# Kernel optimization log

Measured on AMD Instinct MI355X. Metric: run time of the kernel, lower is better.

The kernel has to match this reference:

```python
import jax, jax.numpy as jnp
import numpy as np

N, C, K, M = 100000, 128, 27, 4  # voxels, channels, 3^3 kernel offsets, branches
EPS = 1e-5


def setup_inputs() -> dict:
    key = jax.random.key(0)
    ks = jax.random.split(key, 4)
    x = jax.random.normal(ks[0], (N, C), jnp.float32)
    # neighbor index per voxel per kernel offset (Minkowski kernel map)
    nbr_idx = jax.random.randint(ks[1], (N, K), 0, N, dtype=jnp.int32)
    W1 = jax.random.normal(ks[2], (M, C, C), jnp.float32) * (1.0 / np.sqrt(C))
    g1 = jnp.ones((M, C), jnp.float32)
    b1 = jnp.zeros((M, C), jnp.float32)
    wk = jax.random.normal(ks[3], (M, K, C), jnp.float32) * (1.0 / np.sqrt(K))
    g_out = jnp.ones((C,), jnp.float32)
    b_out = jnp.zeros((C,), jnp.float32)
    return {"x": x, "nbr_idx": nbr_idx, "W1": W1, "g1": g1, "b1": b1,
            "wk": wk, "g_out": g_out, "b_out": b_out}


def _bn(h, g, b):
    # training-mode batch norm over the voxel axis
    mu = h.mean(0)
    var = h.var(0)
    return (h - mu) * jax.lax.rsqrt(var + EPS) * g + b


def reference(x, nbr_idx, W1, g1, b1, wk, g_out, b_out):
    out = jnp.zeros_like(x)
    for m in range(M):  # fixed small branch count
        # Conv1x1 (pointwise) + BN + ReLU
        h = jax.nn.relu(_bn(x @ W1[m], g1[m], b1[m]))  # [N, C]
        # channelwise 3^3 sparse conv: gather neighbor, per-channel scale, accumulate
        acc = jnp.zeros_like(h)
        for k in range(K):  # fixed 27 kernel offsets; avoids [N,K,C] materialization
            acc = acc + h[nbr_idx[:, k]] * wk[m, k]
        out = out + acc  # stack(-1).sum(-1) over branches
    out = jax.nn.relu(_bn(out, g_out, b_out))  # out_bn_relu
    out = out + x  # residual (inplanes == planes)
    return jax.nn.relu(out)  # final nonlinearity ('ReLU')
```

## Files before the change

### kernel.cpp

```cpp
#include <hip/hip_runtime.h>

#define KK 27
#define EPSV 1e-5f

typedef __attribute__((ext_vector_type(8))) short bf16x8;
typedef __attribute__((ext_vector_type(4))) float f32x4;
typedef __attribute__((ext_vector_type(4))) unsigned int u32x4;

static __device__ __forceinline__ unsigned short f2bf(float f) {
    unsigned u = __float_as_uint(f);
    u = u + 0x7fffu + ((u >> 16) & 1u);
    return (unsigned short)(u >> 16);
}
static __device__ __forceinline__ float bflo(unsigned u) { return __uint_as_float(u << 16); }
static __device__ __forceinline__ float bfhi(unsigned u) { return __uint_as_float(u & 0xffff0000u); }

__global__ void k0_wt(const float* __restrict__ W1, unsigned short* __restrict__ WT) {
    int m = blockIdx.x >> 7, n = blockIdx.x & 127, k = threadIdx.x;
    WT[((m * 128 + n) * 128) + k] = f2bf(W1[(m * 128 + k) * 128 + n]);
}

__launch_bounds__(256)
__global__ void kA_gemm(const float* __restrict__ x, const unsigned short* __restrict__ WT,
                        unsigned short* __restrict__ Yall, float* __restrict__ ysum,
                        float* __restrict__ ysq, int N, int m0, int m1, int ystride) {
    __shared__ unsigned short As[64 * 136];
    __shared__ unsigned short Bs[128 * 136];
    const int t = threadIdx.x;
    const int i0 = blockIdx.x * 64;

#pragma unroll
    for (int it = 0; it < 8; ++it) {
        int flat = it * 256 + t;
        int r = flat >> 5, c4 = (flat & 31) * 4;
        float4 v = make_float4(0.f, 0.f, 0.f, 0.f);
        if (i0 + r < N) v = *(const float4*)(x + (size_t)(i0 + r) * 128 + c4);
        ushort4 bb;
        bb.x = f2bf(v.x); bb.y = f2bf(v.y); bb.z = f2bf(v.z); bb.w = f2bf(v.w);
        *(ushort4*)(As + r * 136 + c4) = bb;
    }

    const int w = t >> 6, lane = t & 63;
    const int wr = w >> 1, wc = w & 1;
    const int r16 = lane & 15, q = lane >> 4;

    for (int m = m0; m < m1; ++m) {
        __syncthreads();
        const uint4* Wp = (const uint4*)(WT + (size_t)m * 128 * 128);
#pragma unroll
        for (int it = 0; it < 8; ++it) {
            int flat = it * 256 + t;
            int n = flat >> 4, kc = flat & 15;
            uint4 v = Wp[n * 16 + kc];
            *(uint4*)(Bs + n * 136 + kc * 8) = v;
        }
        __syncthreads();

        f32x4 acc[2][4];
#pragma unroll
        for (int a = 0; a < 2; ++a)
#pragma unroll
            for (int b = 0; b < 4; ++b) { acc[a][b][0] = 0.f; acc[a][b][1] = 0.f; acc[a][b][2] = 0.f; acc[a][b][3] = 0.f; }

#pragma unroll
        for (int ks = 0; ks < 4; ++ks) {
            int ko = ks * 32 + q * 8;
            bf16x8 af[2], bfr[4];
#pragma unroll
            for (int ri = 0; ri < 2; ++ri)
                af[ri] = *(const bf16x8*)(As + (wr * 32 + ri * 16 + r16) * 136 + ko);
#pragma unroll
            for (int ci = 0; ci < 4; ++ci)
                bfr[ci] = *(const bf16x8*)(Bs + (wc * 64 + ci * 16 + r16) * 136 + ko);
#pragma unroll
            for (int ri = 0; ri < 2; ++ri)
#pragma unroll
                for (int ci = 0; ci < 4; ++ci)
                    acc[ri][ci] = __builtin_amdgcn_mfma_f32_16x16x32_bf16(af[ri], bfr[ci], acc[ri][ci], 0, 0, 0);
        }

#pragma unroll
        for (int ci = 0; ci < 4; ++ci) {
            float s = 0.f, s2 = 0.f;
#pragma unroll
            for (int ri = 0; ri < 2; ++ri) {
#pragma unroll
                for (int r = 0; r < 4; ++r) {
                    int row = i0 + wr * 32 + ri * 16 + q * 4 + r;
                    float vv = acc[ri][ci][r];
                    if (row < N) { s += vv; s2 += vv * vv; }
                }
            }
            s  += __shfl_xor(s, 16);  s  += __shfl_xor(s, 32);
            s2 += __shfl_xor(s2, 16); s2 += __shfl_xor(s2, 32);
            if (lane < 16) {
                int col = wc * 64 + ci * 16 + r16;
                atomicAdd(ysum + m * 128 + col, s);
                atomicAdd(ysq  + m * 128 + col, s2);
            }
        }

        __syncthreads();
        unsigned short* Ys = Bs;
#pragma unroll
        for (int ci = 0; ci < 4; ++ci) {
            int col = wc * 64 + ci * 16 + r16;
#pragma unroll
            for (int ri = 0; ri < 2; ++ri) {
#pragma unroll
                for (int r = 0; r < 4; ++r) {
                    int rl = wr * 32 + ri * 16 + q * 4 + r;
                    Ys[rl * 136 + col] = f2bf(acc[ri][ci][r]);
                }
            }
        }
        __syncthreads();
        const int cb = (m - m0) * 128;
#pragma unroll
        for (int it = 0; it < 4; ++it) {
            int chunk = it * 256 + t;
            int row = chunk >> 4, c8 = (chunk & 15) * 8;
            if (i0 + row < N) {
                u32x4 v = *(const u32x4*)(Ys + row * 136 + c8);
                __builtin_nontemporal_store(v, (u32x4*)(Yall + (size_t)(i0 + row) * ystride + cb + c8));
            }
        }
    }
}

__global__ void k2_coef(const float* __restrict__ ysum, const float* __restrict__ ysq,
                        const float* __restrict__ g1, const float* __restrict__ b1,
                        float* __restrict__ a1, float* __restrict__ c1, int N, int m0) {
    int c = threadIdx.x & 127;
    int m = m0 + (threadIdx.x >> 7);
    float mean = ysum[m * 128 + c] / (float)N;
    float var  = ysq[m * 128 + c] / (float)N - mean * mean;
    float a = g1[m * 128 + c] * rsqrtf(var + EPSV);
    a1[m * 128 + c] = a;
    c1[m * 128 + c] = b1[m * 128 + c] - mean * a;
}

__launch_bounds__(256)
__global__ void k4_all(const unsigned short* __restrict__ Yall, const int* __restrict__ nbr,
                       const float* __restrict__ wkg, const float* __restrict__ a1,
                       const float* __restrict__ c1, float* __restrict__ P,
                       float* __restrict__ osum, float* __restrict__ osq, int N) {
    __shared__ unsigned short wkL[4 * KK * 136];
    __shared__ float ssum[128], ssq[128];
    const int t = threadIdx.x;
    for (int idx = t; idx < 4 * KK * 128; idx += 256) {
        int c = idx & 127, km = idx >> 7;
        wkL[km * 136 + c] = f2bf(wkg[idx]);
    }
    if (t < 128) { ssum[t] = 0.f; ssq[t] = 0.f; }

    const int lane = t & 63;
    const int m = lane >> 4, c16 = lane & 15;

    float Ar[8], Cr[8];
    {
        const float4 A0 = *(const float4*)(a1 + m * 128 + c16 * 8);
        const float4 A1 = *(const float4*)(a1 + m * 128 + c16 * 8 + 4);
        const float4 C0 = *(const float4*)(c1 + m * 128 + c16 * 8);
        const float4 C1 = *(const float4*)(c1 + m * 128 + c16 * 8 + 4);
        Ar[0]=A0.x; Ar[1]=A0.y; Ar[2]=A0.z; Ar[3]=A0.w;
        Ar[4]=A1.x; Ar[5]=A1.y; Ar[6]=A1.z; Ar[7]=A1.w;
        Cr[0]=C0.x; Cr[1]=C0.y; Cr[2]=C0.z; Cr[3]=C0.w;
        Cr[4]=C1.x; Cr[5]=C1.y; Cr[6]=C1.z; Cr[7]=C1.w;
    }
    __syncthreads();

    float os[8], oq[8];
#pragma unroll
    for (int e = 0; e < 8; ++e) { os[e] = 0.f; oq[e] = 0.f; }

    const int wid = blockIdx.x * 4 + (t >> 6);
    const int nw  = gridDim.x * 4;
    for (int vox = wid; vox < N; vox += nw) {
        const int sv = __builtin_amdgcn_readfirstlane(vox);
        const int* np = nbr + (size_t)sv * KK;
        float acc[8];
#pragma unroll
        for (int e = 0; e < 8; ++e) acc[e] = 0.f;

#pragma unroll 3
        for (int k = 0; k < KK; ++k) {
            const int j = np[k];
            const uint4 hv = *(const uint4*)(Yall + ((size_t)j << 9) + lane * 8);
            const uint4 wv = *(const uint4*)(wkL + (m * KK + k) * 136 + c16 * 8);
            float h0 = fmaxf(0.f, bflo(hv.x) * Ar[0] + Cr[0]);
            float h1 = fmaxf(0.f, bfhi(hv.x) * Ar[1] + Cr[1]);
            float h2 = fmaxf(0.f, bflo(hv.y) * Ar[2] + Cr[2]);
            float h3 = fmaxf(0.f, bfhi(hv.y) * Ar[3] + Cr[3]);
            float h4 = fmaxf(0.f, bflo(hv.z) * Ar[4] + Cr[4]);
            float h5 = fmaxf(0.f, bfhi(hv.z) * Ar[5] + Cr[5]);
            float h6 = fmaxf(0.f, bflo(hv.w) * Ar[6] + Cr[6]);
            float h7 = fmaxf(0.f, bfhi(hv.w) * Ar[7] + Cr[7]);
            acc[0] += h0 * bflo(wv.x); acc[1] += h1 * bfhi(wv.x);
            acc[2] += h2 * bflo(wv.y); acc[3] += h3 * bfhi(wv.y);
            acc[4] += h4 * bflo(wv.z); acc[5] += h5 * bfhi(wv.z);
            acc[6] += h6 * bflo(wv.w); acc[7] += h7 * bfhi(wv.w);
        }

#pragma unroll
        for (int e = 0; e < 8; ++e) {
            acc[e] += __shfl_xor(acc[e], 16);
            acc[e] += __shfl_xor(acc[e], 32);
        }

        if (lane < 16) {
            f32x4 v0 = {acc[0], acc[1], acc[2], acc[3]};
            f32x4 v1 = {acc[4], acc[5], acc[6], acc[7]};
            float* p = P + (size_t)vox * 128 + c16 * 8;
            __builtin_nontemporal_store(v0, (f32x4*)p);
            __builtin_nontemporal_store(v1, (f32x4*)(p + 4));
#pragma unroll
            for (int e = 0; e < 8; ++e) { os[e] += acc[e]; oq[e] += acc[e] * acc[e]; }
        }
    }

    if (lane < 16) {
#pragma unroll
        for (int e = 0; e < 8; ++e) {
            atomicAdd(ssum + c16 * 8 + e, os[e]);
            atomicAdd(ssq  + c16 * 8 + e, oq[e]);
        }
    }
    __syncthreads();
    if (t < 128) {
        atomicAdd(osum + t, ssum[t]);
        atomicAdd(osq  + t, ssq[t]);
    }
}

template <int MODE>
__launch_bounds__(256)
__global__ void k4_gather(const unsigned short* __restrict__ Ym, int ystride,
                          const int* __restrict__ nbr,
                          const float* __restrict__ wkm, const float* __restrict__ a1m,
                          const float* __restrict__ c1m, float* __restrict__ P,
                          float* __restrict__ osum, float* __restrict__ osq, int N) {
    __shared__ float wkL[KK * 132];
    __shared__ float ssum[128], ssq[128];
    const int t = threadIdx.x;
    for (int idx = t; idx < KK * 128; idx += 256) {
        int k = idx >> 7, c = idx & 127;
        wkL[k * 132 + c] = wkm[k * 128 + c];
    }
    if (MODE == 2) { if (t < 128) { ssum[t] = 0.f; ssq[t] = 0.f; } }

    const int w = t >> 6, lane = t & 63;
    const int q = lane >> 4, c16 = lane & 15;
    const int slot = w * 4 + q;
    const int vox = blockIdx.x * 16 + slot;
    const bool alive = vox < N;

    float aR[8], cR[8];
    {
        const float4 A0 = *(const float4*)(a1m + c16 * 8);
        const float4 A1 = *(const float4*)(a1m + c16 * 8 + 4);
        const float4 C0 = *(const float4*)(c1m + c16 * 8);
        const float4 C1 = *(const float4*)(c1m + c16 * 8 + 4);
        aR[0]=A0.x; aR[1]=A0.y; aR[2]=A0.z; aR[3]=A0.w;
        aR[4]=A1.x; aR[5]=A1.y; aR[6]=A1.z; aR[7]=A1.w;
        cR[0]=C0.x; cR[1]=C0.y; cR[2]=C0.z; cR[3]=C0.w;
        cR[4]=C1.x; cR[5]=C1.y; cR[6]=C1.z; cR[7]=C1.w;
    }
    __syncthreads();

    const long long base = alive ? (long long)vox * KK : 0;
    float acc[8];
#pragma unroll
    for (int e = 0; e < 8; ++e) acc[e] = 0.f;

#pragma unroll 3
    for (int k = 0; k < KK; ++k) {
        int j = nbr[base + k];
        const uint4 hv = *(const uint4*)(Ym + (size_t)j * ystride + c16 * 8);
        const float4 wa = *(const float4*)(wkL + k * 132 + c16 * 8);
        const float4 wb = *(const float4*)(wkL + k * 132 + c16 * 8 + 4);
        float h0 = fmaxf(0.f, bflo(hv.x) * aR[0] + cR[0]);
        float h1 = fmaxf(0.f, bfhi(hv.x) * aR[1] + cR[1]);
        float h2 = fmaxf(0.f, bflo(hv.y) * aR[2] + cR[2]);
        float h3 = fmaxf(0.f, bfhi(hv.y) * aR[3] + cR[3]);
        float h4 = fmaxf(0.f, bflo(hv.z) * aR[4] + cR[4]);
        float h5 = fmaxf(0.f, bfhi(hv.z) * aR[5] + cR[5]);
        float h6 = fmaxf(0.f, bflo(hv.w) * aR[6] + cR[6]);
        float h7 = fmaxf(0.f, bfhi(hv.w) * aR[7] + cR[7]);
        acc[0] += h0 * wa.x; acc[1] += h1 * wa.y;
        acc[2] += h2 * wa.z; acc[3] += h3 * wa.w;
        acc[4] += h4 * wb.x; acc[5] += h5 * wb.y;
        acc[6] += h6 * wb.z; acc[7] += h7 * wb.w;
    }

    float os[8], oq[8];
    if (alive) {
        float* p = P + (size_t)vox * 128 + c16 * 8;
        if (MODE == 0) {
            float4 v0 = {acc[0], acc[1], acc[2], acc[3]};
            float4 v1 = {acc[4], acc[5], acc[6], acc[7]};
            *(float4*)p = v0;
            *(float4*)(p + 4) = v1;
        } else {
            float4 o0 = *(const float4*)p, o1 = *(const float4*)(p + 4);
            o0.x += acc[0]; o0.y += acc[1]; o0.z += acc[2]; o0.w += acc[3];
            o1.x += acc[4]; o1.y += acc[5]; o1.z += acc[6]; o1.w += acc[7];
            *(float4*)p = o0;
            *(float4*)(p + 4) = o1;
            if (MODE == 2) {
                os[0] = o0.x; oq[0] = o0.x * o0.x;
                os[1] = o0.y; oq[1] = o0.y * o0.y;
                os[2] = o0.z; oq[2] = o0.z * o0.z;
                os[3] = o0.w; oq[3] = o0.w * o0.w;
                os[4] = o1.x; oq[4] = o1.x * o1.x;
                os[5] = o1.y; oq[5] = o1.y * o1.y;
                os[6] = o1.z; oq[6] = o1.z * o1.z;
                os[7] = o1.w; oq[7] = o1.w * o1.w;
            }
        }
    }
    if (MODE == 2) {
        if (!alive) {
#pragma unroll
            for (int e = 0; e < 8; ++e) { os[e] = 0.f; oq[e] = 0.f; }
        }
#pragma unroll
        for (int e = 0; e < 8; ++e) {
            os[e] += __shfl_xor(os[e], 16); os[e] += __shfl_xor(os[e], 32);
            oq[e] += __shfl_xor(oq[e], 16); oq[e] += __shfl_xor(oq[e], 32);
        }
        if (lane < 16) {
#pragma unroll
            for (int e = 0; e < 8; ++e) {
                atomicAdd(ssum + c16 * 8 + e, os[e]);
                atomicAdd(ssq  + c16 * 8 + e, oq[e]);
            }
        }
        __syncthreads();
        if (t < 128) {
            atomicAdd(osum + t, ssum[t]);
            atomicAdd(osq  + t, ssq[t]);
        }
    }
}

__global__ void k5_coef(const float* __restrict__ osum, const float* __restrict__ osq,
                        const float* __restrict__ g, const float* __restrict__ b,
                        float* __restrict__ ao, float* __restrict__ co, int N) {
    int c = threadIdx.x;
    float mean = osum[c] / (float)N;
    float var  = osq[c] / (float)N - mean * mean;
    float a = g[c] * rsqrtf(var + EPSV);
    ao[c] = a;
    co[c] = b[c] - mean * a;
}

__launch_bounds__(256)
__global__ void k6_final(float* __restrict__ P, const float* __restrict__ x,
                         const float* __restrict__ ao, const float* __restrict__ co, int N) {
    long long t4 = ((long long)blockIdx.x * 256 + threadIdx.x) * 4;
    if (t4 >= (long long)N * 128) return;
    int c4 = (int)(t4 & 127);
    float4 p  = *(const float4*)(P + t4);
    float4 xv = *(const float4*)(x + t4);
    float4 a  = *(const float4*)(ao + c4);
    float4 c  = *(const float4*)(co + c4);
    float4 o;
    o.x = fmaxf(0.f, fmaxf(0.f, p.x * a.x + c.x) + xv.x);
    o.y = fmaxf(0.f, fmaxf(0.f, p.y * a.y + c.y) + xv.y);
    o.z = fmaxf(0.f, fmaxf(0.f, p.z * a.z + c.z) + xv.z);
    o.w = fmaxf(0.f, fmaxf(0.f, p.w * a.w + c.w) + xv.w);
    *(float4*)(P + t4) = o;
}

extern "C" void kernel_launch(void* const* d_in, const int* in_sizes, int n_in,
                              void* d_out, int out_size, void* d_ws, size_t ws_size,
                              hipStream_t stream) {
    const float* x     = (const float*)d_in[0];
    const int*   nbr   = (const int*)d_in[1];
    const float* W1    = (const float*)d_in[2];
    const float* g1    = (const float*)d_in[3];
    const float* b1    = (const float*)d_in[4];
    const float* wk    = (const float*)d_in[5];
    const float* g_out = (const float*)d_in[6];
    const float* b_out = (const float*)d_in[7];
    const int N = in_sizes[0] / 128;

    float* P = (float*)d_out;
    char* ws = (char*)d_ws;
    float* ysum = (float*)ws;
    float* ysq  = ysum + 512;
    float* osum = ysq + 512;
    float* osq  = osum + 128;
    float* a1   = osq + 128;
    float* c1   = a1 + 512;
    float* ao   = c1 + 512;
    float* co   = ao + 128;
    unsigned short* WT = (unsigned short*)(ws + 16384);
    unsigned short* Y  = (unsigned short*)(ws + 16384 + 131072);

    const bool fused = ws_size >= (size_t)16384 + 131072 + (size_t)N * 512 * 2;

    hipMemsetAsync(d_ws, 0, 5120, stream);
    k0_wt<<<512, 128, 0, stream>>>(W1, WT);

    const int gA = (N + 63) / 64;
    const int g4 = (N + 15) / 16;

    if (fused) {
        kA_gemm<<<gA, 256, 0, stream>>>(x, WT, Y, ysum, ysq, N, 0, 4, 512);
        k2_coef<<<1, 512, 0, stream>>>(ysum, ysq, g1, b1, a1, c1, N, 0);
        k4_all<<<2048, 256, 0, stream>>>(Y, nbr, wk, a1, c1, P, osum, osq, N);
    } else {
        for (int m = 0; m < 4; ++m) {
            kA_gemm<<<gA, 256, 0, stream>>>(x, WT, Y, ysum, ysq, N, m, m + 1, 128);
            k2_coef<<<1, 128, 0, stream>>>(ysum, ysq, g1, b1, a1, c1, N, m);
            if (m == 0)
                k4_gather<0><<<g4, 256, 0, stream>>>(Y, 128, nbr, wk + m * KK * 128,
                                                     a1 + m * 128, c1 + m * 128, P, osum, osq, N);
            else if (m == 3)
                k4_gather<2><<<g4, 256, 0, stream>>>(Y, 128, nbr, wk + m * KK * 128,
                                                     a1 + m * 128, c1 + m * 128, P, osum, osq, N);
            else
                k4_gather<1><<<g4, 256, 0, stream>>>(Y, 128, nbr, wk + m * KK * 128,
                                                     a1 + m * 128, c1 + m * 128, P, osum, osq, N);
        }
    }
    k5_coef<<<1, 128, 0, stream>>>(osum, osq, g_out, b_out, ao, co, N);
    const int g6 = (int)(((long long)N * 128 / 4 + 255) / 256);
    k6_final<<<g6, 256, 0, stream>>>(P, x, ao, co, N);
}
```

Before: 629.1 us.

## Precompute BN+ReLU into fp16 activations and process voxel pairs in gather

```diff
diff --git a/kernel.cpp b/kernel.cpp
--- a/kernel.cpp
+++ b/kernel.cpp
@@ -12,8 +12,20 @@
     u = u + 0x7fffu + ((u >> 16) & 1u);
     return (unsigned short)(u >> 16);
 }
-static __device__ __forceinline__ float bflo(unsigned u) { return __uint_as_float(u << 16); }
-static __device__ __forceinline__ float bfhi(unsigned u) { return __uint_as_float(u & 0xffff0000u); }
+
+static __device__ __forceinline__ unsigned short f2h(float f) {
+    _Float16 h = (_Float16)f;
+    unsigned short u;
+    __builtin_memcpy(&u, &h, 2);
+    return u;
+}
+static __device__ __forceinline__ float h2f(unsigned short s) {
+    _Float16 h;
+    __builtin_memcpy(&h, &s, 2);
+    return (float)h;
+}
+static __device__ __forceinline__ float hlo(unsigned u) { return h2f((unsigned short)(u & 0xffffu)); }
+static __device__ __forceinline__ float hhi(unsigned u) { return h2f((unsigned short)(u >> 16)); }
 
 __global__ void k0_wt(const float* __restrict__ W1, unsigned short* __restrict__ WT) {
     int m = blockIdx.x >> 7, n = blockIdx.x & 127, k = threadIdx.x;
@@ -110,7 +122,7 @@
 #pragma unroll
                 for (int r = 0; r < 4; ++r) {
                     int rl = wr * 32 + ri * 16 + q * 4 + r;
-                    Ys[rl * 136 + col] = f2bf(acc[ri][ci][r]);
+                    Ys[rl * 136 + col] = f2h(acc[ri][ci][r]);
                 }
             }
         }
@@ -141,34 +153,50 @@
 }
 
 __launch_bounds__(256)
-__global__ void k4_all(const unsigned short* __restrict__ Yall, const int* __restrict__ nbr,
-                       const float* __restrict__ wkg, const float* __restrict__ a1,
-                       const float* __restrict__ c1, float* __restrict__ P,
+__global__ void kH_bn(unsigned short* __restrict__ Y, const float* __restrict__ a1,
+                      const float* __restrict__ c1, int N) {
+    long long i = (long long)blockIdx.x * 256 + threadIdx.x;
+    if (i >= (long long)N * 64) return;
+    const int e0 = ((int)i & 63) * 8;
+    uint4 v = *(const uint4*)(Y + (i << 3));
+    const float4 A0 = *(const float4*)(a1 + e0);
+    const float4 A1 = *(const float4*)(a1 + e0 + 4);
+    const float4 C0 = *(const float4*)(c1 + e0);
+    const float4 C1 = *(const float4*)(c1 + e0 + 4);
+    float h0 = fmaxf(0.f, hlo(v.x) * A0.x + C0.x);
+    float h1 = fmaxf(0.f, hhi(v.x) * A0.y + C0.y);
+    float h2 = fmaxf(0.f, hlo(v.y) * A0.z + C0.z);
+    float h3 = fmaxf(0.f, hhi(v.y) * A0.w + C0.w);
+    float h4 = fmaxf(0.f, hlo(v.z) * A1.x + C1.x);
+    float h5 = fmaxf(0.f, hhi(v.z) * A1.y + C1.y);
+    float h6 = fmaxf(0.f, hlo(v.w) * A1.z + C1.z);
+    float h7 = fmaxf(0.f, hhi(v.w) * A1.w + C1.w);
+    uint4 o;
+    o.x = (unsigned)f2h(h0) | ((unsigned)f2h(h1) << 16);
+    o.y = (unsigned)f2h(h2) | ((unsigned)f2h(h3) << 16);
+    o.z = (unsigned)f2h(h4) | ((unsigned)f2h(h5) << 16);
+    o.w = (unsigned)f2h(h6) | ((unsigned)f2h(h7) << 16);
+    *(uint4*)(Y + (i << 3)) = o;
+}
+
+__launch_bounds__(256)
+__global__ void k4_all(const unsigned short* __restrict__ H, const int* __restrict__ nbr,
+                       const float* __restrict__ wkg, float* __restrict__ P,
                        float* __restrict__ osum, float* __restrict__ osq, int N) {
     __shared__ unsigned short wkL[4 * KK * 136];
     __shared__ float ssum[128], ssq[128];
     const int t = threadIdx.x;
     for (int idx = t; idx < 4 * KK * 128; idx += 256) {
         int c = idx & 127, km = idx >> 7;
-        wkL[km * 136 + c] = f2bf(wkg[idx]);
+        wkL[km * 136 + c] = f2h(wkg[idx]);
     }
     if (t < 128) { ssum[t] = 0.f; ssq[t] = 0.f; }
+    __syncthreads();
 
     const int lane = t & 63;
     const int m = lane >> 4, c16 = lane & 15;
-
-    float Ar[8], Cr[8];
-    {
-        const float4 A0 = *(const float4*)(a1 + m * 128 + c16 * 8);
-        const float4 A1 = *(const float4*)(a1 + m * 128 + c16 * 8 + 4);
-        const float4 C0 = *(const float4*)(c1 + m * 128 + c16 * 8);
-        const float4 C1 = *(const float4*)(c1 + m * 128 + c16 * 8 + 4);
-        Ar[0]=A0.x; Ar[1]=A0.y; Ar[2]=A0.z; Ar[3]=A0.w;
-        Ar[4]=A1.x; Ar[5]=A1.y; Ar[6]=A1.z; Ar[7]=A1.w;
-        Cr[0]=C0.x; Cr[1]=C0.y; Cr[2]=C0.z; Cr[3]=C0.w;
-        Cr[4]=C1.x; Cr[5]=C1.y; Cr[6]=C1.z; Cr[7]=C1.w;
-    }
-    __syncthreads();
+    const unsigned short* wbase = wkL + (m * KK) * 136 + c16 * 8;
+    const unsigned short* hbase = H + lane * 8;
 
     float os[8], oq[8];
 #pragma unroll
@@ -176,50 +204,58 @@
 
     const int wid = blockIdx.x * 4 + (t >> 6);
     const int nw  = gridDim.x * 4;
-    for (int vox = wid; vox < N; vox += nw) {
-        const int sv = __builtin_amdgcn_readfirstlane(vox);
-        const int* np = nbr + (size_t)sv * KK;
-        float acc[8];
-#pragma unroll
-        for (int e = 0; e < 8; ++e) acc[e] = 0.f;
+    const int npair = (N + 1) >> 1;
+    for (int vp = wid; vp < npair; vp += nw) {
+        const int v0 = __builtin_amdgcn_readfirstlane(vp * 2);
+        const bool has1 = (v0 + 1) < N;
+        const int* np0 = nbr + (size_t)v0 * KK;
+        const int* np1 = np0 + (has1 ? KK : 0);
+        float acc0[8], acc1[8];
+#pragma unroll
+        for (int e = 0; e < 8; ++e) { acc0[e] = 0.f; acc1[e] = 0.f; }
 
 #pragma unroll 3
         for (int k = 0; k < KK; ++k) {
-            const int j = np[k];
-            const uint4 hv = *(const uint4*)(Yall + ((size_t)j << 9) + lane * 8);
-            const uint4 wv = *(const uint4*)(wkL + (m * KK + k) * 136 + c16 * 8);
-            float h0 = fmaxf(0.f, bflo(hv.x) * Ar[0] + Cr[0]);
-            float h1 = fmaxf(0.f, bfhi(hv.x) * Ar[1] + Cr[1]);
-            float h2 = fmaxf(0.f, bflo(hv.y) * Ar[2] + Cr[2]);
-            float h3 = fmaxf(0.f, bfhi(hv.y) * Ar[3] + Cr[3]);
-            float h4 = fmaxf(0.f, bflo(hv.z) * Ar[4] + Cr[4]);
-            float h5 = fmaxf(0.f, bfhi(hv.z) * Ar[5] + Cr[5]);
-            float h6 = fmaxf(0.f, bflo(hv.w) * Ar[6] + Cr[6]);
-            float h7 = fmaxf(0.f, bfhi(hv.w) * Ar[7] + Cr[7]);
-            acc[0] += h0 * bflo(wv.x); acc[1] += h1 * bfhi(wv.x);
-            acc[2] += h2 * bflo(wv.y); acc[3] += h3 * bfhi(wv.y);
-            acc[4] += h4 * bflo(wv.z); acc[5] += h5 * bfhi(wv.z);
-            acc[6] += h6 * bflo(wv.w); acc[7] += h7 * bfhi(wv.w);
+            const int j0 = np0[k];
+            const int j1 = np1[k];
+            const uint4 h0v = *(const uint4*)(hbase + ((size_t)j0 << 9));
+            const uint4 h1v = *(const uint4*)(hbase + ((size_t)j1 << 9));
+            const uint4 wv  = *(const uint4*)(wbase + k * 136);
+            const float w0 = hlo(wv.x), w1 = hhi(wv.x), w2 = hlo(wv.y), w3 = hhi(wv.y);
+            const float w4 = hlo(wv.z), w5 = hhi(wv.z), w6 = hlo(wv.w), w7 = hhi(wv.w);
+            acc0[0] += hlo(h0v.x) * w0; acc0[1] += hhi(h0v.x) * w1;
+            acc0[2] += hlo(h0v.y) * w2; acc0[3] += hhi(h0v.y) * w3;
+            acc0[4] += hlo(h0v.z) * w4; acc0[5] += hhi(h0v.z) * w5;
+            acc0[6] += hlo(h0v.w) * w6; acc0[7] += hhi(h0v.w) * w7;
+            acc1[0] += hlo(h1v.x) * w0; acc1[1] += hhi(h1v.x) * w1;
+            acc1[2] += hlo(h1v.y) * w2; acc1[3] += hhi(h1v.y) * w3;
+            acc1[4] += hlo(h1v.z) * w4; acc1[5] += hhi(h1v.z) * w5;
+            acc1[6] += hlo(h1v.w) * w6; acc1[7] += hhi(h1v.w) * w7;
         }
 
 #pragma unroll
         for (int e = 0; e < 8; ++e) {
-            acc[e] += __shfl_xor(acc[e], 16);
-            acc[e] += __shfl_xor(acc[e], 32);
-        }
-
-        if (lane < 16) {
-            f32x4 v0 = {acc[0], acc[1], acc[2], acc[3]};
-            f32x4 v1 = {acc[4], acc[5], acc[6], acc[7]};
-            float* p = P + (size_t)vox * 128 + c16 * 8;
-            __builtin_nontemporal_store(v0, (f32x4*)p);
-            __builtin_nontemporal_store(v1, (f32x4*)(p + 4));
-#pragma unroll
-            for (int e = 0; e < 8; ++e) { os[e] += acc[e]; oq[e] += acc[e] * acc[e]; }
-        }
-    }
-
-    if (lane < 16) {
+            acc0[e] += __shfl_xor(acc0[e], 16);
+            acc0[e] += __shfl_xor(acc0[e], 32);
+            acc1[e] += __shfl_xor(acc1[e], 16);
+            acc1[e] += __shfl_xor(acc1[e], 32);
+        }
+        const int q = lane >> 4;
+        if (q == 0 || (q == 1 && has1)) {
+            float av[8];
+#pragma unroll
+            for (int e = 0; e < 8; ++e) av[e] = (q == 0) ? acc0[e] : acc1[e];
+            f32x4 x0 = {av[0], av[1], av[2], av[3]};
+            f32x4 x1 = {av[4], av[5], av[6], av[7]};
+            float* p = P + (size_t)(v0 + q) * 128 + c16 * 8;
+            __builtin_nontemporal_store(x0, (f32x4*)p);
+            __builtin_nontemporal_store(x1, (f32x4*)(p + 4));
+#pragma unroll
+            for (int e = 0; e < 8; ++e) { os[e] += av[e]; oq[e] += av[e] * av[e]; }
+        }
+    }
+
+    if ((lane >> 4) < 2) {
 #pragma unroll
         for (int e = 0; e < 8; ++e) {
             atomicAdd(ssum + c16 * 8 + e, os[e]);
@@ -279,14 +315,14 @@
         const uint4 hv = *(const uint4*)(Ym + (size_t)j * ystride + c16 * 8);
         const float4 wa = *(const float4*)(wkL + k * 132 + c16 * 8);
         const float4 wb = *(const float4*)(wkL + k * 132 + c16 * 8 + 4);
-        float h0 = fmaxf(0.f, bflo(hv.x) * aR[0] + cR[0]);
-        float h1 = fmaxf(0.f, bfhi(hv.x) * aR[1] + cR[1]);
-        float h2 = fmaxf(0.f, bflo(hv.y) * aR[2] + cR[2]);
-        float h3 = fmaxf(0.f, bfhi(hv.y) * aR[3] + cR[3]);
-        float h4 = fmaxf(0.f, bflo(hv.z) * aR[4] + cR[4]);
-        float h5 = fmaxf(0.f, bfhi(hv.z) * aR[5] + cR[5]);
-        float h6 = fmaxf(0.f, bflo(hv.w) * aR[6] + cR[6]);
-        float h7 = fmaxf(0.f, bfhi(hv.w) * aR[7] + cR[7]);
+        float h0 = fmaxf(0.f, hlo(hv.x) * aR[0] + cR[0]);
+        float h1 = fmaxf(0.f, hhi(hv.x) * aR[1] + cR[1]);
+        float h2 = fmaxf(0.f, hlo(hv.y) * aR[2] + cR[2]);
+        float h3 = fmaxf(0.f, hhi(hv.y) * aR[3] + cR[3]);
+        float h4 = fmaxf(0.f, hlo(hv.z) * aR[4] + cR[4]);
+        float h5 = fmaxf(0.f, hhi(hv.z) * aR[5] + cR[5]);
+        float h6 = fmaxf(0.f, hlo(hv.w) * aR[6] + cR[6]);
+        float h7 = fmaxf(0.f, hhi(hv.w) * aR[7] + cR[7]);
         acc[0] += h0 * wa.x; acc[1] += h1 * wa.y;
         acc[2] += h2 * wa.z; acc[3] += h3 * wa.w;
         acc[4] += h4 * wb.x; acc[5] += h5 * wb.y;
@@ -410,7 +446,10 @@
     if (fused) {
         kA_gemm<<<gA, 256, 0, stream>>>(x, WT, Y, ysum, ysq, N, 0, 4, 512);
         k2_coef<<<1, 512, 0, stream>>>(ysum, ysq, g1, b1, a1, c1, N, 0);
-        k4_all<<<2048, 256, 0, stream>>>(Y, nbr, wk, a1, c1, P, osum, osq, N);
+        const long long chunks = (long long)N * 64;
+        const int gH = (int)((chunks + 255) / 256);
+        kH_bn<<<gH, 256, 0, stream>>>(Y, a1, c1, N);
+        k4_all<<<2048, 256, 0, stream>>>(Y, nbr, wk, P, osum, osq, N);
     } else {
         for (int m = 0; m < 4; ++m) {
             kA_gemm<<<gA, 256, 0, stream>>>(x, WT, Y, ysum, ysq, N, m, m + 1, 128);
```

Result: slower. 660.2 us (+4.9%).
